# Kernel tuning notes

Measured on AMD Instinct MI355X. Metric: run time of the kernel, lower is better.

The kernel has to match this reference:

```python
import jax, jax.numpy as jnp
import numpy as np

# model constants (from source: PRE/COMM/OUT sizes; chosen: G, D, E, T, NF)
G, D, E, T = 128, 64, 8, 4096          # group feats, per-elevator feats, n elevators, timesteps
PRE, CI, CH, OUT, NF = 256, 128, 128, 128, 64
ROUNDS, DROPOFF = 3, 0.333
IN = G + D                              # elevator_input_size = 192
OIN = 2 * CH + IN                       # out-LSTM input = 448


def _cell(x, h, c, Wih, Whh, b):
    # torch nn.LSTM cell, gate order i,f,g,o; b = b_ih + b_hh
    g = x @ Wih.T + h @ Whh.T + b
    i, f, gg, o = jnp.split(g, 4, axis=-1)
    c2 = jax.nn.sigmoid(f) * c + jax.nn.sigmoid(i) * jnp.tanh(gg)
    h2 = jax.nn.sigmoid(o) * jnp.tanh(c2)
    return h2, c2


def _forward(features, pre_h0, pre_c0, out_h0, out_c0,
             Wih_p0, Whh_p0, b_p0, Wih_p1, Whh_p1, b_p1, Wfc, bfc,
             Wih_c0, Whh_c0, b_c0, Wih_c1, Whh_c1, b_c1,
             Wih_o, Whh_o, b_o, Wtar, btar, Wdir, bdir):
    def step(carry, feat):
        pre_h, pre_c, out_h, out_c = carry
        group = feat[:G]
        ele = feat[G:].reshape(E, D)
        x = jnp.concatenate([jnp.broadcast_to(group, (E, G)), ele], axis=-1)  # [E, IN]
        # preprocess: 2-layer LSTM single step, batched over elevators
        h0, c0 = _cell(x, pre_h[:, 0], pre_c[:, 0], Wih_p0, Whh_p0, b_p0)
        h1, c1 = _cell(h0, pre_h[:, 1], pre_c[:, 1], Wih_p1, Whh_p1, b_p1)
        pre_out = jax.nn.leaky_relu(h1 @ Wfc.T + bfc, 0.05)                   # [E, CI]
        new_pre_h = jnp.stack([h0, h1], axis=1)
        new_pre_c = jnp.stack([c0, c1], axis=1)
        # alpha-decayed communication rounds: sequential scan over elevators
        ch = jnp.zeros((2, CH), jnp.float32)
        cc = jnp.zeros((2, CH), jnp.float32)
        alpha = 1.0
        for _ in range(ROUNDS):
            def comm_step(cs, xin, alpha=alpha):
                ch_, cc_ = cs
                h0n, c0n = _cell(xin, ch_[0], cc_[0], Wih_c0, Whh_c0, b_c0)
                h0b = (1.0 - alpha) * ch_[0] + alpha * h0n
                c0b = (1.0 - alpha) * cc_[0] + alpha * c0n
                h1n, c1n = _cell(h0b, ch_[1], cc_[1], Wih_c1, Whh_c1, b_c1)
                h1b = (1.0 - alpha) * ch_[1] + alpha * h1n
                c1b = (1.0 - alpha) * cc_[1] + alpha * c1n
                return (jnp.stack([h0b, h1b]), jnp.stack([c0b, c1b])), None
            (ch, cc), _ = jax.lax.scan(comm_step, (ch, cc), pre_out)
            alpha *= DROPOFF
        group_dec = cc.reshape(-1)                                            # [2*CH] = comm_c.flatten()
        out_in = jnp.concatenate([jnp.broadcast_to(group_dec, (E, 2 * CH)), x], axis=-1)  # [E, OIN]
        oh, oc = _cell(out_in, out_h, out_c, Wih_o, Whh_o, b_o)
        tar = jax.nn.softmax(oh @ Wtar.T + btar, axis=-1)                     # [E, NF]
        dr = jax.nn.softmax(oh @ Wdir.T + bdir, axis=-1)                      # [E, 3]
        return (new_pre_h, new_pre_c, oh, oc), (tar, dr)

    _, (tar_seq, dir_seq) = jax.lax.scan(step, (pre_h0, pre_c0, out_h0, out_c0), features)
    return tar_seq, dir_seq


def setup_inputs() -> dict:
    key = jax.random.key(0)
    ks = iter(jax.random.split(key, 32))
    p = lambda *s: jax.random.normal(next(ks), s, jnp.float32) * 0.05
    return {
        "features": jax.random.normal(next(ks), (T, G + E * D), jnp.float32),
        "pre_h0": jnp.zeros((E, 2, PRE), jnp.float32),
        "pre_c0": jnp.zeros((E, 2, PRE), jnp.float32),
        "out_h0": jnp.zeros((E, OUT), jnp.float32),
        "out_c0": jnp.zeros((E, OUT), jnp.float32),
        "Wih_p0": p(4 * PRE, IN), "Whh_p0": p(4 * PRE, PRE), "b_p0": p(4 * PRE),
        "Wih_p1": p(4 * PRE, PRE), "Whh_p1": p(4 * PRE, PRE), "b_p1": p(4 * PRE),
        "Wfc": p(CI, PRE), "bfc": p(CI),
        "Wih_c0": p(4 * CH, CI), "Whh_c0": p(4 * CH, CH), "b_c0": p(4 * CH),
        "Wih_c1": p(4 * CH, CH), "Whh_c1": p(4 * CH, CH), "b_c1": p(4 * CH),
        "Wih_o": p(4 * OUT, OIN), "Whh_o": p(4 * OUT, OUT), "b_o": p(4 * OUT),
        "Wtar": p(NF, OUT), "btar": p(NF),
        "Wdir": p(3, OUT), "bdir": p(3),
    }


def reference(features, pre_h0, pre_c0, out_h0, out_c0,
              Wih_p0, Whh_p0, b_p0, Wih_p1, Whh_p1, b_p1, Wfc, bfc,
              Wih_c0, Whh_c0, b_c0, Wih_c1, Whh_c1, b_c1,
              Wih_o, Whh_o, b_o, Wtar, btar, Wdir, bdir):
    return _forward(features, pre_h0, pre_c0, out_h0, out_c0,
                    Wih_p0, Whh_p0, b_p0, Wih_p1, Whh_p1, b_p1, Wfc, bfc,
                    Wih_c0, Whh_c0, b_c0, Wih_c1, Whh_c1, b_c1,
                    Wih_o, Whh_o, b_o, Wtar, btar, Wdir, bdir)
```

## Files before the change

### kernel.cpp

```cpp
#include <hip/hip_runtime.h>
#include <hip/hip_bf16.h>

#define T_   4096
#define E_   8
#define NCON 176

typedef unsigned long long ull;

__device__ __forceinline__ float sigm(float x)  { return 1.0f / (1.0f + __expf(-x)); }
__device__ __forceinline__ float tanh_(float x) { return 1.0f - 2.0f / (__expf(2.0f * x) + 1.0f); }

__device__ __forceinline__ ull aload64(const ull* p) {
  return __hip_atomic_load(p, __ATOMIC_RELAXED, __HIP_MEMORY_SCOPE_AGENT);
}
__device__ __forceinline__ int aload32(const int* p) {
  return __hip_atomic_load(p, __ATOMIC_RELAXED, __HIP_MEMORY_SCOPE_AGENT);
}
__device__ __forceinline__ float aloadf(const float* p) {
  return __hip_atomic_load(p, __ATOMIC_RELAXED, __HIP_MEMORY_SCOPE_AGENT);
}
__device__ __forceinline__ void lbar() {
  asm volatile("s_waitcnt lgkmcnt(0)\n\ts_barrier" ::: "memory");
}

#define FMA_8(ACC, W, VA, VB)                                   \
  ACC[0] = fmaf((W), (VA).x, ACC[0]); ACC[1] = fmaf((W), (VA).y, ACC[1]); \
  ACC[2] = fmaf((W), (VA).z, ACC[2]); ACC[3] = fmaf((W), (VA).w, ACC[3]); \
  ACC[4] = fmaf((W), (VB).x, ACC[4]); ACC[5] = fmaf((W), (VB).y, ACC[5]); \
  ACC[6] = fmaf((W), (VB).z, ACC[6]); ACC[7] = fmaf((W), (VB).w, ACC[7]);

__global__ void initK(const float* __restrict__ Wih_p0, const float* __restrict__ Whh_p0,
                      const float* __restrict__ Wih_p1, const float* __restrict__ Whh_p1,
                      const float* __restrict__ Wih_c0, const float* __restrict__ Whh_c0,
                      const float* __restrict__ Wih_c1, const float* __restrict__ Whh_c1,
                      const float* __restrict__ Wih_o,
                      float* wt_p0, float* wt_p1, float* wt_c0, float* wt_c1,
                      float* wt_o1, float* wt_o2, int* flags) {
  const int NW = 458752 + 524288 + 131072 + 131072 + 131072 + 98304;
  const int NF = 2 * 64 * 32 * 32 + 512 * 32;
  const int NTOT = NW + NF;
  const int gsz = gridDim.x * blockDim.x;
  for (int i = blockIdx.x * blockDim.x + threadIdx.x; i < NTOT; i += gsz) {
    int idx = i;
    if (idx < 458752) { int k = idx >> 10, c = idx & 1023;
      int wg = c >> 5, r5 = c & 31, gate = r5 >> 3, jl = r5 & 7;
      int col = gate * 256 + wg * 8 + jl;
      wt_p0[idx] = (k < 192) ? Wih_p0[col * 192 + k] : Whh_p0[col * 256 + (k - 192)]; continue; }
    idx -= 458752;
    if (idx < 524288) { int k = idx >> 10, c = idx & 1023;
      int wg = c >> 5, r5 = c & 31, gate = r5 >> 3, jl = r5 & 7;
      int col = gate * 256 + wg * 8 + jl;
      wt_p1[idx] = (k < 256) ? Wih_p1[col * 256 + k] : Whh_p1[col * 256 + (k - 256)]; continue; }
    idx -= 524288;
    if (idx < 131072) { int k = idx >> 9, r = idx & 511;
      wt_c0[idx] = (k < 128) ? Wih_c0[r * 128 + k] : Whh_c0[r * 128 + (k - 128)]; continue; }
    idx -= 131072;
    if (idx < 131072) { int k = idx >> 9, r = idx & 511;
      wt_c1[idx] = (k < 128) ? Wih_c1[r * 128 + k] : Whh_c1[r * 128 + (k - 128)]; continue; }
    idx -= 131072;
    if (idx < 131072) { int k = idx >> 9, r = idx & 511;
      wt_o1[idx] = Wih_o[r * 448 + k]; continue; }
    idx -= 131072;
    if (idx < 98304) { int k = idx >> 9, r = idx & 511;
      wt_o2[idx] = Wih_o[r * 448 + 256 + k]; continue; }
    idx -= 98304;
    flags[idx] = 0;
  }
}

__global__ void opre2K(const float* __restrict__ feat, const float* __restrict__ wt_o2,
                       __hip_bfloat16* __restrict__ opre2) {
  __shared__ float xb[192 * 8];
  const int t = blockIdx.x, tid = threadIdx.x;
  const float* ft = feat + (size_t)t * 640;
  for (int idx = tid; idx < 192 * 8; idx += 256) {
    int k = idx >> 3, e = idx & 7;
    xb[idx] = (k < 128) ? ft[k] : ft[128 + e * 64 + (k - 128)];
  }
  __syncthreads();
  const int r = tid;
  float A0[8] = {0,0,0,0,0,0,0,0};
  float A1[8] = {0,0,0,0,0,0,0,0};
  const float4* x4 = (const float4*)xb;
  #pragma unroll 2
  for (int k = 0; k < 192; ++k) {
    float w0 = wt_o2[k * 512 + r];
    float w1 = wt_o2[k * 512 + 256 + r];
    float4 a = x4[k * 2], b = x4[k * 2 + 1];
    FMA_8(A0, w0, a, b);
    FMA_8(A1, w1, a, b);
  }
  #pragma unroll
  for (int e = 0; e < 8; ++e) {
    opre2[((size_t)t * 8 + e) * 512 + r]       = __float2bfloat16(A0[e]);
    opre2[((size_t)t * 8 + e) * 512 + 256 + r] = __float2bfloat16(A1[e]);
  }
}

__device__ __forceinline__ void comm_cell(
    const float* __restrict__ wt, const float* __restrict__ bias,
    const float* xin, float* hL, float* cL, float* glb, float* hout,
    float alpha, int tid) {
  const int r = tid;
  float A0[8] = {0,0,0,0,0,0,0,0};
  float A1[8] = {0,0,0,0,0,0,0,0};
  const float4* x4 = (const float4*)xin;
  #pragma unroll 2
  for (int k = 0; k < 128; ++k) {
    float w0 = wt[k * 512 + r];
    float w1 = wt[k * 512 + 256 + r];
    float4 a = x4[k * 2], b = x4[k * 2 + 1];
    FMA_8(A0, w0, a, b);
    FMA_8(A1, w1, a, b);
  }
  const float4* h4 = (const float4*)hL;
  #pragma unroll 2
  for (int k = 0; k < 128; ++k) {
    float w0 = wt[(128 + k) * 512 + r];
    float w1 = wt[(128 + k) * 512 + 256 + r];
    float4 a = h4[k * 2], b = h4[k * 2 + 1];
    FMA_8(A0, w0, a, b);
    FMA_8(A1, w1, a, b);
  }
  {
    float4* g4 = (float4*)glb;
    g4[r * 2]             = make_float4(A0[0], A0[1], A0[2], A0[3]);
    g4[r * 2 + 1]         = make_float4(A0[4], A0[5], A0[6], A0[7]);
    g4[(256 + r) * 2]     = make_float4(A1[0], A1[1], A1[2], A1[3]);
    g4[(256 + r) * 2 + 1] = make_float4(A1[4], A1[5], A1[6], A1[7]);
  }
  __syncthreads();
  for (int idx = tid; idx < 1024; idx += 256) {
    int jj = idx >> 3, tt = idx & 7;
    float gi = glb[jj * 8 + tt]         + bias[jj];
    float gf = glb[(128 + jj) * 8 + tt] + bias[128 + jj];
    float gg = glb[(256 + jj) * 8 + tt] + bias[256 + jj];
    float go = glb[(384 + jj) * 8 + tt] + bias[384 + jj];
    float cold = cL[idx], hold = hL[idx];
    float c2 = sigm(gf) * cold + sigm(gi) * tanh_(gg);
    float h2 = sigm(go) * tanh_(c2);
    float hb = fmaf(alpha, h2 - hold, hold);
    float cb = fmaf(alpha, c2 - cold, cold);
    hL[idx] = hb; cL[idx] = cb;
    if (hout) hout[idx] = hb;
  }
  __syncthreads();
}

__launch_bounds__(256, 1)
__global__ void megaK(const float* __restrict__ feat,
                      const float* __restrict__ pre_h0, const float* __restrict__ pre_c0,
                      const float* __restrict__ wt_p0, const float* __restrict__ wt_p1,
                      const float* __restrict__ b_p0, const float* __restrict__ b_p1,
                      float* __restrict__ h0ring, float* __restrict__ h1ring,
                      float* __restrict__ h1all,
                      int* __restrict__ flagsA, int* __restrict__ flagsB,
                      const float* __restrict__ Wfc, const float* __restrict__ bfc,
                      const float* __restrict__ wt_c0, const float* __restrict__ wt_c1,
                      const float* __restrict__ b_c0, const float* __restrict__ b_c1,
                      const float* __restrict__ wt_o1, const float* __restrict__ b_o,
                      float* __restrict__ opre1, int* __restrict__ flagC,
                      const __hip_bfloat16* __restrict__ opre2,
                      const float* __restrict__ Whh_o, const float* __restrict__ out_h0,
                      const float* __restrict__ out_c0, float* __restrict__ oh_g) {
  __shared__ float lds[38912];
  const int wg = blockIdx.x, tid = threadIdx.x;

  if (wg < 32) {
    float* wl   = lds;
    float* xbuf = lds + 14336;
    float* hsf  = lds + 15872;
    float* gl   = lds + 17920;
    const int r5 = tid & 31, kq = tid >> 5;
    for (int idx = tid; idx < 14336; idx += 256)
      wl[idx] = wt_p0[(size_t)(idx >> 5) * 1024 + wg * 32 + (idx & 31)];
    float creg = 0.f, bi = 0.f, bff = 0.f, bg = 0.f, bo = 0.f;
    if (tid < 64) {
      const int jl = tid >> 3, e = tid & 7, j = wg * 8 + jl;
      creg = pre_c0[(e * 2 + 0) * 256 + j];
      bi = b_p0[j]; bff = b_p0[256 + j]; bg = b_p0[512 + j]; bo = b_p0[768 + j];
    }
    for (int idx = tid; idx < 2048; idx += 256) {
      int k = idx >> 3, e = idx & 7;
      hsf[idx] = pre_h0[(e * 2 + 0) * 256 + k];
    }
    for (int idx = tid; idx < 1536; idx += 256) {
      int k = idx >> 3, e = idx & 7;
      xbuf[idx] = (k < 128) ? feat[k] : feat[128 + e * 64 + (k - 128)];
    }
    __syncthreads();
    float Ax[8] = {0,0,0,0,0,0,0,0};
    {
      const float4* x4 = (const float4*)xbuf;
      #pragma unroll
      for (int k = kq * 24; k < kq * 24 + 24; ++k) {
        float w = wl[k * 32 + r5];
        float4 a = x4[k * 2], b = x4[k * 2 + 1];
        FMA_8(Ax, w, a, b);
      }
    }
    for (int t = 0; t < T_; ++t) {
      float px[6];
      if (t + 1 < T_) {
        const float* ft1 = feat + (size_t)(t + 1) * 640;
        #pragma unroll
        for (int i = 0; i < 6; ++i) {
          int idx = tid + i * 256; int k = idx >> 3, e = idx & 7;
          px[i] = (k < 128) ? ft1[k] : ft1[128 + e * 64 + (k - 128)];
        }
      }
      float A[8];
      #pragma unroll
      for (int i = 0; i < 8; ++i) A[i] = Ax[i];
      {
        const float4* h4 = (const float4*)hsf;
        #pragma unroll
        for (int k2 = 0; k2 < 32; ++k2) {
          const int k = kq * 32 + k2;
          float w = wl[(192 + k) * 32 + r5];
          float4 a = h4[k * 2], b = h4[k * 2 + 1];
          FMA_8(A, w, a, b);
        }
      }
      {
        float4* g4 = (float4*)gl;
        g4[(kq * 32 + r5) * 2]     = make_float4(A[0], A[1], A[2], A[3]);
        g4[(kq * 32 + r5) * 2 + 1] = make_float4(A[4], A[5], A[6], A[7]);
      }
      if (tid >= 224 && t >= 8) {
        const int* fp = flagsB + ((size_t)((t - 8) & 63) * 32 + (tid - 224)) * 32;
        while (aload32(fp) < t - 7) __builtin_amdgcn_s_sleep(1);
      }
      lbar();
      if (tid < 64) {
        float s0 = 0.f, s1 = 0.f, s2 = 0.f, s3 = 0.f;
        #pragma unroll
        for (int q = 0; q < 8; ++q) {
          s0 += gl[q * 256 + tid];       s1 += gl[q * 256 + 64 + tid];
          s2 += gl[q * 256 + 128 + tid]; s3 += gl[q * 256 + 192 + tid];
        }
        float c2 = sigm(s1 + bff) * creg + sigm(s0 + bi) * tanh_(s2 + bg);
        float h2 = sigm(s3 + bo) * tanh_(c2);
        creg = c2;
        __hip_atomic_store(&h0ring[(size_t)(t & 7) * 2048 + wg * 64 + tid], h2,
                           __ATOMIC_RELAXED, __HIP_MEMORY_SCOPE_AGENT);
        asm volatile("s_waitcnt vmcnt(0)" ::: "memory");
        if (tid == 0)
          __hip_atomic_store(&flagsA[((size_t)(t & 63) * 32 + wg) * 32], t + 1,
                             __ATOMIC_RELAXED, __HIP_MEMORY_SCOPE_AGENT);
      }
      if (t + 1 >= T_) break;
      #pragma unroll
      for (int i = 0; i < 6; ++i) xbuf[tid + i * 256] = px[i];
      if (tid >= 64 && tid < 96) {
        const int* fp = flagsA + ((size_t)(t & 63) * 32 + (tid - 64)) * 32;
        while (aload32(fp) < t + 1) __builtin_amdgcn_s_sleep(1);
      }
      lbar();
      ull v[4];
      {
        const ull* s8 = (const ull*)(h0ring + (size_t)(t & 7) * 2048);
        #pragma unroll
        for (int i = 0; i < 4; ++i) v[i] = aload64(s8 + tid * 4 + i);
      }
      #pragma unroll
      for (int i = 0; i < 8; ++i) Ax[i] = 0.f;
      {
        const float4* x4 = (const float4*)xbuf;
        #pragma unroll
        for (int k = kq * 24; k < kq * 24 + 24; ++k) {
          float w = wl[k * 32 + r5];
          float4 a = x4[k * 2], b = x4[k * 2 + 1];
          FMA_8(Ax, w, a, b);
        }
      }
      {
        ull* d8 = (ull*)hsf;
        #pragma unroll
        for (int i = 0; i < 4; ++i) d8[tid * 4 + i] = v[i];
      }
      lbar();
    }
  } else if (wg < 64) {
    const int wgl = wg - 32;
    float* wl  = lds;
    float* xh0 = lds + 16384;
    float* hsf = lds + 18432;
    float* gl  = lds + 20480;
    const int r5 = tid & 31, kq = tid >> 5;
    for (int idx = tid; idx < 16384; idx += 256)
      wl[idx] = wt_p1[(size_t)(idx >> 5) * 1024 + wgl * 32 + (idx & 31)];
    float creg = 0.f, bi = 0.f, bff = 0.f, bg = 0.f, bo = 0.f;
    if (tid < 64) {
      const int jl = tid >> 3, e = tid & 7, j = wgl * 8 + jl;
      creg = pre_c0[(e * 2 + 1) * 256 + j];
      bi = b_p1[j]; bff = b_p1[256 + j]; bg = b_p1[512 + j]; bo = b_p1[768 + j];
    }
    for (int idx = tid; idx < 2048; idx += 256) {
      int k = idx >> 3, e = idx & 7;
      hsf[idx] = pre_h0[(e * 2 + 1) * 256 + k];
    }
    __syncthreads();
    if (tid >= 64 && tid < 128) {
      const int lane = tid - 64;
      const int slot = lane >> 5, b = lane & 31;
      const int* fp = flagsA + ((size_t)slot * 32 + b) * 32;
      while (aload32(fp) < slot + 1) __builtin_amdgcn_s_sleep(1);
    }
    __syncthreads();
    ull v0[4];
    {
      const ull* s8 = (const ull*)h0ring;
      #pragma unroll
      for (int i = 0; i < 4; ++i) v0[i] = aload64(s8 + tid * 4 + i);
    }
    {
      ull* d8 = (ull*)xh0;
      #pragma unroll
      for (int i = 0; i < 4; ++i) d8[tid * 4 + i] = v0[i];
    }
    lbar();
    float Ax[8] = {0,0,0,0,0,0,0,0};
    {
      const float4* x4 = (const float4*)xh0;
      #pragma unroll
      for (int k = kq * 32; k < kq * 32 + 32; ++k) {
        float w = wl[k * 32 + r5];
        float4 a = x4[k * 2], b = x4[k * 2 + 1];
        FMA_8(Ax, w, a, b);
      }
    }
    {
      const ull* s8 = (const ull*)(h0ring + 2048);
      #pragma unroll
      for (int i = 0; i < 4; ++i) v0[i] = aload64(s8 + tid * 4 + i);
    }
    for (int t = 0; t < T_; ++t) {
      float A[8];
      #pragma unroll
      for (int i = 0; i < 8; ++i) A[i] = Ax[i];
      {
        const float4* h4 = (const float4*)hsf;
        #pragma unroll
        for (int k2 = 0; k2 < 32; ++k2) {
          const int k = kq * 32 + k2;
          float w = wl[(256 + k) * 32 + r5];
          float4 a = h4[k * 2], b = h4[k * 2 + 1];
          FMA_8(A, w, a, b);
        }
      }
      {
        float4* g4 = (float4*)gl;
        g4[(kq * 32 + r5) * 2]     = make_float4(A[0], A[1], A[2], A[3]);
        g4[(kq * 32 + r5) * 2 + 1] = make_float4(A[4], A[5], A[6], A[7]);
      }
      lbar();
      if (tid < 64) {
        float s0 = 0.f, s1 = 0.f, s2 = 0.f, s3 = 0.f;
        #pragma unroll
        for (int q = 0; q < 8; ++q) {
          s0 += gl[q * 256 + tid];       s1 += gl[q * 256 + 64 + tid];
          s2 += gl[q * 256 + 128 + tid]; s3 += gl[q * 256 + 192 + tid];
        }
        float c2 = sigm(s1 + bff) * creg + sigm(s0 + bi) * tanh_(s2 + bg);
        float h2 = sigm(s3 + bo) * tanh_(c2);
        creg = c2;
        __hip_atomic_store(&h1ring[(size_t)(t & 7) * 2048 + wgl * 64 + tid], h2,
                           __ATOMIC_RELAXED, __HIP_MEMORY_SCOPE_AGENT);
        __hip_atomic_store(&h1all[(size_t)t * 2048 + wgl * 64 + tid], h2,
                           __ATOMIC_RELAXED, __HIP_MEMORY_SCOPE_AGENT);
        asm volatile("s_waitcnt vmcnt(0)" ::: "memory");
        if (tid == 0)
          __hip_atomic_store(&flagsB[((size_t)(t & 63) * 32 + wgl) * 32], t + 1,
                             __ATOMIC_RELAXED, __HIP_MEMORY_SCOPE_AGENT);
      }
      if (t + 1 >= T_) break;
      if (tid >= 64 && tid < 128) {
        const int lane = tid - 64;
        if (lane < 32) {
          const int* fp = flagsB + ((size_t)(t & 63) * 32 + lane) * 32;
          while (aload32(fp) < t + 1) __builtin_amdgcn_s_sleep(1);
        } else if (t + 2 < T_) {
          const int* fp = flagsA + ((size_t)((t + 2) & 63) * 32 + (lane - 32)) * 32;
          while (aload32(fp) < t + 3) __builtin_amdgcn_s_sleep(1);
        }
      }
      lbar();
      ull v1[4];
      {
        const ull* s8 = (const ull*)(h1ring + (size_t)(t & 7) * 2048);
        #pragma unroll
        for (int i = 0; i < 4; ++i) v1[i] = aload64(s8 + tid * 4 + i);
      }
      {
        ull* d8 = (ull*)xh0;
        #pragma unroll
        for (int i = 0; i < 4; ++i) d8[tid * 4 + i] = v0[i];
      }
      lbar();
      if (t + 2 < T_) {
        const ull* s8 = (const ull*)(h0ring + (size_t)((t + 2) & 7) * 2048);
        #pragma unroll
        for (int i = 0; i < 4; ++i) v0[i] = aload64(s8 + tid * 4 + i);
      }
      #pragma unroll
      for (int i = 0; i < 8; ++i) Ax[i] = 0.f;
      {
        const float4* x4 = (const float4*)xh0;
        #pragma unroll
        for (int k = kq * 32; k < kq * 32 + 32; ++k) {
          float w = wl[k * 32 + r5];
          float4 a = x4[k * 2], b = x4[k * 2 + 1];
          FMA_8(Ax, w, a, b);
        }
      }
      {
        ull* d8 = (ull*)hsf;
        #pragma unroll
        for (int i = 0; i < 4; ++i) d8[tid * 4 + i] = v1[i];
      }
      lbar();
    }
  } else if (wg < 72) {
    const int e = wg - 64;
    float* wlds = lds;
    float* ohl  = lds + 32768;
    float* gl   = lds + 32896;
    for (int idx = tid; idx < 32768; idx += 256) {
      int k = idx >> 8, rr = idx & 255;
      wlds[idx] = Whh_o[(256 + rr) * 128 + k];
    }
    float w[128];
    #pragma unroll
    for (int k = 0; k < 128; ++k) w[k] = Whh_o[tid * 128 + k];
    if (tid < 128) ohl[tid] = out_h0[e * 128 + tid];
    float creg = (tid < 128) ? out_c0[e * 128 + tid] : 0.f;
    __syncthreads();
    if (tid == 0) { while (aload32(&flagC[0]) == 0) __builtin_amdgcn_s_sleep(4); }
    __syncthreads();
    const int r0 = tid, r1 = tid + 256;
    float pa = aloadf(&opre1[r0]), pb = aloadf(&opre1[r1]);
    float qa = __bfloat162float(opre2[(size_t)e * 512 + r0]);
    float qb = __bfloat162float(opre2[(size_t)e * 512 + r1]);
    float na = aloadf(&opre1[512 + r0]), nb = aloadf(&opre1[512 + r1]);
    float ma = __bfloat162float(opre2[(size_t)(8 + e) * 512 + r0]);
    float mb = __bfloat162float(opre2[(size_t)(8 + e) * 512 + r1]);
    for (int t = 0; t < T_; ++t) {
      float a0 = pa + qa, a1 = pb + qb;
      pa = na; pb = nb; qa = ma; qb = mb;
      if ((t & 7) == 6 && t + 2 < T_) {
        if (tid == 0) { while (aload32(&flagC[((t + 2) >> 3) * 32]) == 0) __builtin_amdgcn_s_sleep(4); }
        __syncthreads();
      }
      if (t + 2 < T_) {
        na = aloadf(&opre1[(size_t)(t + 2) * 512 + r0]);
        nb = aloadf(&opre1[(size_t)(t + 2) * 512 + r1]);
        ma = __bfloat162float(opre2[((size_t)(t + 2) * 8 + e) * 512 + r0]);
        mb = __bfloat162float(opre2[((size_t)(t + 2) * 8 + e) * 512 + r1]);
      }
      const float4* o4 = (const float4*)ohl;
      #pragma unroll
      for (int kk = 0; kk < 32; ++kk) {
        float4 x = o4[kk];
        a0 = fmaf(w[kk * 4 + 0], x.x, a0); a0 = fmaf(w[kk * 4 + 1], x.y, a0);
        a0 = fmaf(w[kk * 4 + 2], x.z, a0); a0 = fmaf(w[kk * 4 + 3], x.w, a0);
        a1 = fmaf(wlds[(kk * 4 + 0) * 256 + tid], x.x, a1);
        a1 = fmaf(wlds[(kk * 4 + 1) * 256 + tid], x.y, a1);
        a1 = fmaf(wlds[(kk * 4 + 2) * 256 + tid], x.z, a1);
        a1 = fmaf(wlds[(kk * 4 + 3) * 256 + tid], x.w, a1);
      }
      gl[r0] = a0; gl[r1] = a1;
      __syncthreads();
      if (tid < 128) {
        float gi = gl[tid], gf = gl[128 + tid], gg = gl[256 + tid], go = gl[384 + tid];
        float c2 = sigm(gf) * creg + sigm(gi) * tanh_(gg);
        float h2 = sigm(go) * tanh_(c2);
        creg = c2;
        ohl[tid] = h2;
        oh_g[(size_t)t * 1024 + e * 128 + tid] = h2;
      }
      __syncthreads();
    }
  } else {
    const int cb = wg - 72;
    float* h1c    = lds;
    float* polAll = lds + 16384;
    float* ch0 = lds + 24576; float* cc0 = lds + 25600;
    float* ch1 = lds + 26624; float* cc1 = lds + 27648;
    float* h0b = lds + 28672;
    float* glb = lds + 29696;
    for (int chunk = cb; chunk < 512; chunk += NCON) {
      const int t0 = chunk * 8;
      if (tid < 32) {
        const int* fp = flagsB + ((size_t)((t0 + 7) & 63) * 32 + tid) * 32;
        while (aload32(fp) < t0 + 8) __builtin_amdgcn_s_sleep(4);
      }
      __syncthreads();
      {
        const ull* src = (const ull*)(h1all + (size_t)t0 * 2048);
        ull* dst = (ull*)h1c;
        for (int i = tid; i < 8192; i += 256) dst[i] = aload64(src + i);
      }
      __syncthreads();
      {
        const int c = tid >> 1, half = tid & 1;
        const float bv = bfc[c];
        const float* wrow = Wfc + c * 256;
        for (int tt = 0; tt < 8; ++tt) {
          float a0 = bv, a1 = bv, a2 = bv, a3 = bv;
          const float4* h4 = (const float4*)(h1c + tt * 2048);
          #pragma unroll 4
          for (int k = 0; k < 256; ++k) {
            float wv = wrow[k];
            float4 x = h4[k * 2 + half];
            a0 = fmaf(wv, x.x, a0); a1 = fmaf(wv, x.y, a1);
            a2 = fmaf(wv, x.z, a2); a3 = fmaf(wv, x.w, a3);
          }
          float vv[4] = {a0, a1, a2, a3};
          #pragma unroll
          for (int i = 0; i < 4; ++i) {
            float v = vv[i];
            v = (v > 0.f) ? v : 0.05f * v;
            polAll[(half * 4 + i) * 1024 + c * 8 + tt] = v;
          }
        }
      }
      for (int idx = tid; idx < 1024; idx += 256) { ch0[idx]=0.f; cc0[idx]=0.f; ch1[idx]=0.f; cc1[idx]=0.f; }
      __syncthreads();
      float alpha = 1.0f;
      for (int rd = 0; rd < 3; ++rd) {
        for (int e = 0; e < E_; ++e) {
          comm_cell(wt_c0, b_c0, polAll + e * 1024, ch0, cc0, glb, h0b, alpha, tid);
          comm_cell(wt_c1, b_c1, h0b, ch1, cc1, glb, nullptr, alpha, tid);
        }
        alpha *= 0.333f;
      }
      {
        const int r = tid;
        float A0[8], A1[8];
        #pragma unroll
        for (int tt = 0; tt < 8; ++tt) { A0[tt] = b_o[r]; A1[tt] = b_o[256 + r]; }
        const float4* c04 = (const float4*)cc0;
        const float4* c14 = (const float4*)cc1;
        #pragma unroll 2
        for (int k = 0; k < 128; ++k) {
          float w0 = wt_o1[k * 512 + r], w1 = wt_o1[k * 512 + 256 + r];
          float4 a = c04[k * 2], b = c04[k * 2 + 1];
          FMA_8(A0, w0, a, b);
          FMA_8(A1, w1, a, b);
        }
        #pragma unroll 2
        for (int k = 0; k < 128; ++k) {
          float w0 = wt_o1[(128 + k) * 512 + r], w1 = wt_o1[(128 + k) * 512 + 256 + r];
          float4 a = c14[k * 2], b = c14[k * 2 + 1];
          FMA_8(A0, w0, a, b);
          FMA_8(A1, w1, a, b);
        }
        #pragma unroll
        for (int tt = 0; tt < 8; ++tt) {
          __hip_atomic_store(&opre1[((size_t)(t0 + tt)) * 512 + r], A0[tt],
                             __ATOMIC_RELAXED, __HIP_MEMORY_SCOPE_AGENT);
          __hip_atomic_store(&opre1[((size_t)(t0 + tt)) * 512 + 256 + r], A1[tt],
                             __ATOMIC_RELAXED, __HIP_MEMORY_SCOPE_AGENT);
        }
      }
      __syncthreads();
      if (tid == 0)
        __hip_atomic_store(&flagC[chunk * 32], 1, __ATOMIC_RELAXED, __HIP_MEMORY_SCOPE_AGENT);
      __syncthreads();
    }
  }
}

__global__ void phaseD(const float* __restrict__ oh_g,
                       const float* __restrict__ Wtar, const float* __restrict__ btar,
                       const float* __restrict__ Wdir, const float* __restrict__ bdir,
                       float* __restrict__ outp) {
  __shared__ float ohl[1024];
  const int t = blockIdx.x, tid = threadIdx.x;
  for (int idx = tid; idx < 1024; idx += 64) ohl[idx] = oh_g[(size_t)t * 1024 + idx];
  __syncthreads();
  const int f = tid;
  for (int e = 0; e < E_; ++e) {
    float acc = btar[f];
    const float* wr = Wtar + f * 128;
    #pragma unroll 4
    for (int k = 0; k < 128; ++k) acc = fmaf(wr[k], ohl[e * 128 + k], acc);
    float m = acc;
    #pragma unroll
    for (int off = 32; off; off >>= 1) m = fmaxf(m, __shfl_xor(m, off, 64));
    float ex = __expf(acc - m);
    float s = ex;
    #pragma unroll
    for (int off = 32; off; off >>= 1) s += __shfl_xor(s, off, 64);
    outp[((size_t)t * 8 + e) * 64 + f] = ex / s;
  }
  if (tid < 8) {
    int e = tid;
    float d0 = bdir[0], d1 = bdir[1], d2 = bdir[2];
    #pragma unroll 4
    for (int k = 0; k < 128; ++k) {
      float x = ohl[e * 128 + k];
      d0 = fmaf(Wdir[k], x, d0);
      d1 = fmaf(Wdir[128 + k], x, d1);
      d2 = fmaf(Wdir[256 + k], x, d2);
    }
    float m = fmaxf(d0, fmaxf(d1, d2));
    float x0 = __expf(d0 - m), x1 = __expf(d1 - m), x2 = __expf(d2 - m);
    float s = x0 + x1 + x2;
    float* dp = outp + (size_t)T_ * 8 * 64 + ((size_t)t * 8 + e) * 3;
    dp[0] = x0 / s; dp[1] = x1 / s; dp[2] = x2 / s;
  }
}

extern "C" void kernel_launch(void* const* d_in, const int* in_sizes, int n_in,
                              void* d_out, int out_size, void* d_ws, size_t ws_size,
                              hipStream_t stream) {
  (void)in_sizes; (void)n_in; (void)out_size; (void)ws_size;
  const float* feat   = (const float*)d_in[0];
  const float* pre_h0 = (const float*)d_in[1];
  const float* pre_c0 = (const float*)d_in[2];
  const float* out_h0 = (const float*)d_in[3];
  const float* out_c0 = (const float*)d_in[4];
  const float* Wih_p0 = (const float*)d_in[5];
  const float* Whh_p0 = (const float*)d_in[6];
  const float* b_p0   = (const float*)d_in[7];
  const float* Wih_p1 = (const float*)d_in[8];
  const float* Whh_p1 = (const float*)d_in[9];
  const float* b_p1   = (const float*)d_in[10];
  const float* Wfc    = (const float*)d_in[11];
  const float* bfc    = (const float*)d_in[12];
  const float* Wih_c0 = (const float*)d_in[13];
  const float* Whh_c0 = (const float*)d_in[14];
  const float* b_c0   = (const float*)d_in[15];
  const float* Wih_c1 = (const float*)d_in[16];
  const float* Whh_c1 = (const float*)d_in[17];
  const float* b_c1   = (const float*)d_in[18];
  const float* Wih_o  = (const float*)d_in[19];
  const float* Whh_o  = (const float*)d_in[20];
  const float* b_o    = (const float*)d_in[21];
  const float* Wtar   = (const float*)d_in[22];
  const float* btar   = (const float*)d_in[23];
  const float* Wdir   = (const float*)d_in[24];
  const float* bdir   = (const float*)d_in[25];
  float* outp = (float*)d_out;

  float* ws = (float*)d_ws;
  size_t off = 0;
  float* opre1    = ws + off; off += (size_t)T_ * 512;
  float* oh_g     = ws + off; off += (size_t)T_ * E_ * 128;
  float* wt_p0    = ws + off; off += (size_t)448 * 1024;
  float* wt_p1    = ws + off; off += (size_t)512 * 1024;
  float* wt_c0    = ws + off; off += (size_t)256 * 512;
  float* wt_c1    = ws + off; off += (size_t)256 * 512;
  float* wt_o1    = ws + off; off += (size_t)256 * 512;
  float* wt_o2    = ws + off; off += (size_t)192 * 512;
  __hip_bfloat16* opre2 = (__hip_bfloat16*)(ws + off);
  off += (size_t)T_ * E_ * 512 / 2;
  float* h1all  = ws + off; off += (size_t)T_ * 2048;
  float* h0ring = ws + off; off += (size_t)8 * 2048;
  float* h1ring = ws + off; off += (size_t)8 * 2048;
  int* flags    = (int*)(ws + off);
  int* flagsA   = flags;
  int* flagsB   = flags + (size_t)64 * 32 * 32;
  int* flagC    = flags + (size_t)2 * 64 * 32 * 32;

  initK<<<dim3(1024), dim3(256), 0, stream>>>(
      Wih_p0, Whh_p0, Wih_p1, Whh_p1, Wih_c0, Whh_c0, Wih_c1, Whh_c1, Wih_o,
      wt_p0, wt_p1, wt_c0, wt_c1, wt_o1, wt_o2, flags);
  opre2K<<<dim3(T_), dim3(256), 0, stream>>>(feat, wt_o2, opre2);
  megaK<<<dim3(32 + 32 + 8 + NCON), dim3(256), 0, stream>>>(
      feat, pre_h0, pre_c0, wt_p0, wt_p1, b_p0, b_p1,
      h0ring, h1ring, h1all, flagsA, flagsB,
      Wfc, bfc, wt_c0, wt_c1, b_c0, b_c1, wt_o1, b_o, opre1, flagC,
      opre2, Whh_o, out_h0, out_c0, oh_g);
  phaseD<<<dim3(T_), dim3(64), 0, stream>>>(oh_g, Wtar, btar, Wdir, bdir, outp);
}
```

Before: 16.66 ms.

## Replace per-step flag handshakes with sequence-tagged ring entries between LSTM layers

Each h value written to the inter-workgroup rings is packed with its timestep tag in a 64-bit word, so consumers poll the data itself instead of waiting on separate flagsA counters. The vmcnt drain and flag store after every step disappear, and each block skips reloading its own slice by writing it straight to LDS. The h0 ring grows to 32 slots and the layer-1 backpressure flag is published only every 8 steps, loosening the coupling between producers and consumers. This doubles ring traffic and relies on 64-bit atomic loads being untorn and on the wider ring staying ahead of readers.

```diff
diff --git a/kernel.cpp b/kernel.cpp
--- a/kernel.cpp
+++ b/kernel.cpp
@@ -35,10 +35,10 @@
                       const float* __restrict__ Wih_c1, const float* __restrict__ Whh_c1,
                       const float* __restrict__ Wih_o,
                       float* wt_p0, float* wt_p1, float* wt_c0, float* wt_c1,
-                      float* wt_o1, float* wt_o2, int* flags) {
+                      float* wt_o1, float* wt_o2, int* zbase) {
   const int NW = 458752 + 524288 + 131072 + 131072 + 131072 + 98304;
-  const int NF = 2 * 64 * 32 * 32 + 512 * 32;
-  const int NTOT = NW + NF;
+  const int NZ = 131072 + 32768 + 65536 + 16384;
+  const int NTOT = NW + NZ;
   const int gsz = gridDim.x * blockDim.x;
   for (int i = blockIdx.x * blockDim.x + threadIdx.x; i < NTOT; i += gsz) {
     int idx = i;
@@ -64,7 +64,7 @@
     if (idx < 98304) { int k = idx >> 9, r = idx & 511;
       wt_o2[idx] = Wih_o[r * 448 + 256 + k]; continue; }
     idx -= 98304;
-    flags[idx] = 0;
+    zbase[idx] = 0;
   }
 }
 
@@ -152,9 +152,9 @@
                       const float* __restrict__ pre_h0, const float* __restrict__ pre_c0,
                       const float* __restrict__ wt_p0, const float* __restrict__ wt_p1,
                       const float* __restrict__ b_p0, const float* __restrict__ b_p1,
-                      float* __restrict__ h0ring, float* __restrict__ h1ring,
+                      ull* __restrict__ h0ring, ull* __restrict__ h1ring,
                       float* __restrict__ h1all,
-                      int* __restrict__ flagsA, int* __restrict__ flagsB,
+                      int* __restrict__ flagsB,
                       const float* __restrict__ Wfc, const float* __restrict__ bfc,
                       const float* __restrict__ wt_c0, const float* __restrict__ wt_c1,
                       const float* __restrict__ b_c0, const float* __restrict__ b_c1,
@@ -189,6 +189,7 @@
       xbuf[idx] = (k < 128) ? feat[k] : feat[128 + e * 64 + (k - 128)];
     }
     __syncthreads();
+    const bool own = ((tid >> 3) == wg);
     float Ax[8] = {0,0,0,0,0,0,0,0};
     {
       const float4* x4 = (const float4*)xbuf;
@@ -227,9 +228,10 @@
         g4[(kq * 32 + r5) * 2]     = make_float4(A[0], A[1], A[2], A[3]);
         g4[(kq * 32 + r5) * 2 + 1] = make_float4(A[4], A[5], A[6], A[7]);
       }
-      if (tid >= 224 && t >= 8) {
-        const int* fp = flagsB + ((size_t)((t - 8) & 63) * 32 + (tid - 224)) * 32;
-        while (aload32(fp) < t - 7) __builtin_amdgcn_s_sleep(1);
+      if (t >= 24 && tid >= 224) {
+        const int t2 = (t - 24) | 7;
+        const int* fp = flagsB + ((size_t)(t2 & 63) * 32 + (tid - 224)) * 32;
+        while (aload32(fp) < t2 + 1) __builtin_amdgcn_s_sleep(1);
       }
       lbar();
       if (tid < 64) {
@@ -242,26 +244,20 @@
         float c2 = sigm(s1 + bff) * creg + sigm(s0 + bi) * tanh_(s2 + bg);
         float h2 = sigm(s3 + bo) * tanh_(c2);
         creg = c2;
-        __hip_atomic_store(&h0ring[(size_t)(t & 7) * 2048 + wg * 64 + tid], h2,
+        ull pk = ((ull)(unsigned)(t + 1) << 32) | (ull)__float_as_uint(h2);
+        __hip_atomic_store(&h0ring[(size_t)(t & 31) * 2048 + wg * 64 + tid], pk,
                            __ATOMIC_RELAXED, __HIP_MEMORY_SCOPE_AGENT);
-        asm volatile("s_waitcnt vmcnt(0)" ::: "memory");
-        if (tid == 0)
-          __hip_atomic_store(&flagsA[((size_t)(t & 63) * 32 + wg) * 32], t + 1,
-                             __ATOMIC_RELAXED, __HIP_MEMORY_SCOPE_AGENT);
+        hsf[wg * 64 + tid] = h2;
       }
       if (t + 1 >= T_) break;
       #pragma unroll
       for (int i = 0; i < 6; ++i) xbuf[tid + i * 256] = px[i];
-      if (tid >= 64 && tid < 96) {
-        const int* fp = flagsA + ((size_t)(t & 63) * 32 + (tid - 64)) * 32;
-        while (aload32(fp) < t + 1) __builtin_amdgcn_s_sleep(1);
-      }
       lbar();
-      ull v[4];
-      {
-        const ull* s8 = (const ull*)(h0ring + (size_t)(t & 7) * 2048);
-        #pragma unroll
-        for (int i = 0; i < 4; ++i) v[i] = aload64(s8 + tid * 4 + i);
+      ull v[8];
+      const ull* rp = h0ring + (size_t)(t & 31) * 2048 + tid * 8;
+      if (!own) {
+        #pragma unroll
+        for (int i = 0; i < 8; ++i) v[i] = aload64(rp + i);
       }
       #pragma unroll
       for (int i = 0; i < 8; ++i) Ax[i] = 0.f;
@@ -274,10 +270,24 @@
           FMA_8(Ax, w, a, b);
         }
       }
-      {
-        ull* d8 = (ull*)hsf;
-        #pragma unroll
-        for (int i = 0; i < 4; ++i) d8[tid * 4 + i] = v[i];
+      if (!own) {
+        const unsigned want = (unsigned)(t + 1);
+        while (true) {
+          bool ok = true;
+          #pragma unroll
+          for (int i = 0; i < 8; ++i) ok &= ((unsigned)(v[i] >> 32) == want);
+          if (ok) break;
+          __builtin_amdgcn_s_sleep(1);
+          #pragma unroll
+          for (int i = 0; i < 8; ++i) v[i] = aload64(rp + i);
+        }
+        float4* h4w = (float4*)hsf;
+        h4w[tid * 2] = make_float4(
+            __uint_as_float((unsigned)v[0]), __uint_as_float((unsigned)v[1]),
+            __uint_as_float((unsigned)v[2]), __uint_as_float((unsigned)v[3]));
+        h4w[tid * 2 + 1] = make_float4(
+            __uint_as_float((unsigned)v[4]), __uint_as_float((unsigned)v[5]),
+            __uint_as_float((unsigned)v[6]), __uint_as_float((unsigned)v[7]));
       }
       lbar();
     }
@@ -301,23 +311,28 @@
       hsf[idx] = pre_h0[(e * 2 + 1) * 256 + k];
     }
     __syncthreads();
-    if (tid >= 64 && tid < 128) {
-      const int lane = tid - 64;
-      const int slot = lane >> 5, b = lane & 31;
-      const int* fp = flagsA + ((size_t)slot * 32 + b) * 32;
-      while (aload32(fp) < slot + 1) __builtin_amdgcn_s_sleep(1);
-    }
-    __syncthreads();
-    ull v0[4];
+    const bool own = ((tid >> 3) == wgl);
+    float pv[8];
     {
-      const ull* s8 = (const ull*)h0ring;
-      #pragma unroll
-      for (int i = 0; i < 4; ++i) v0[i] = aload64(s8 + tid * 4 + i);
-    }
-    {
-      ull* d8 = (ull*)xh0;
-      #pragma unroll
-      for (int i = 0; i < 4; ++i) d8[tid * 4 + i] = v0[i];
+      ull v[8];
+      const ull* rp = h0ring + tid * 8;
+      #pragma unroll
+      for (int i = 0; i < 8; ++i) v[i] = aload64(rp + i);
+      while (true) {
+        bool ok = true;
+        #pragma unroll
+        for (int i = 0; i < 8; ++i) ok &= ((unsigned)(v[i] >> 32) == 1u);
+        if (ok) break;
+        __builtin_amdgcn_s_sleep(1);
+        #pragma unroll
+        for (int i = 0; i < 8; ++i) v[i] = aload64(rp + i);
+      }
+      ((float4*)xh0)[tid * 2] = make_float4(
+          __uint_as_float((unsigned)v[0]), __uint_as_float((unsigned)v[1]),
+          __uint_as_float((unsigned)v[2]), __uint_as_float((unsigned)v[3]));
+      ((float4*)xh0)[tid * 2 + 1] = make_float4(
+          __uint_as_float((unsigned)v[4]), __uint_as_float((unsigned)v[5]),
+          __uint_as_float((unsigned)v[6]), __uint_as_float((unsigned)v[7]));
     }
     lbar();
     float Ax[8] = {0,0,0,0,0,0,0,0};
@@ -331,9 +346,21 @@
       }
     }
     {
-      const ull* s8 = (const ull*)(h0ring + 2048);
-      #pragma unroll
-      for (int i = 0; i < 4; ++i) v0[i] = aload64(s8 + tid * 4 + i);
+      ull v[8];
+      const ull* rp = h0ring + 2048 + tid * 8;
+      #pragma unroll
+      for (int i = 0; i < 8; ++i) v[i] = aload64(rp + i);
+      while (true) {
+        bool ok = true;
+        #pragma unroll
+        for (int i = 0; i < 8; ++i) ok &= ((unsigned)(v[i] >> 32) == 2u);
+        if (ok) break;
+        __builtin_amdgcn_s_sleep(1);
+        #pragma unroll
+        for (int i = 0; i < 8; ++i) v[i] = aload64(rp + i);
+      }
+      #pragma unroll
+      for (int i = 0; i < 8; ++i) pv[i] = __uint_as_float((unsigned)v[i]);
     }
     for (int t = 0; t < T_; ++t) {
       float A[8];
@@ -365,43 +392,34 @@
         float c2 = sigm(s1 + bff) * creg + sigm(s0 + bi) * tanh_(s2 + bg);
         float h2 = sigm(s3 + bo) * tanh_(c2);
         creg = c2;
-        __hip_atomic_store(&h1ring[(size_t)(t & 7) * 2048 + wgl * 64 + tid], h2,
+        ull pk = ((ull)(unsigned)(t + 1) << 32) | (ull)__float_as_uint(h2);
+        __hip_atomic_store(&h1ring[(size_t)(t & 7) * 2048 + wgl * 64 + tid], pk,
                            __ATOMIC_RELAXED, __HIP_MEMORY_SCOPE_AGENT);
         __hip_atomic_store(&h1all[(size_t)t * 2048 + wgl * 64 + tid], h2,
                            __ATOMIC_RELAXED, __HIP_MEMORY_SCOPE_AGENT);
-        asm volatile("s_waitcnt vmcnt(0)" ::: "memory");
-        if (tid == 0)
-          __hip_atomic_store(&flagsB[((size_t)(t & 63) * 32 + wgl) * 32], t + 1,
-                             __ATOMIC_RELAXED, __HIP_MEMORY_SCOPE_AGENT);
+        hsf[wgl * 64 + tid] = h2;
+        if ((t & 7) == 7) {
+          asm volatile("s_waitcnt vmcnt(0)" ::: "memory");
+          if (tid == 0)
+            __hip_atomic_store(&flagsB[((size_t)(t & 63) * 32 + wgl) * 32], t + 1,
+                               __ATOMIC_RELAXED, __HIP_MEMORY_SCOPE_AGENT);
+        }
       }
       if (t + 1 >= T_) break;
-      if (tid >= 64 && tid < 128) {
-        const int lane = tid - 64;
-        if (lane < 32) {
-          const int* fp = flagsB + ((size_t)(t & 63) * 32 + lane) * 32;
-          while (aload32(fp) < t + 1) __builtin_amdgcn_s_sleep(1);
-        } else if (t + 2 < T_) {
-          const int* fp = flagsA + ((size_t)((t + 2) & 63) * 32 + (lane - 32)) * 32;
-          while (aload32(fp) < t + 3) __builtin_amdgcn_s_sleep(1);
-        }
-      }
+      ((float4*)xh0)[tid * 2]     = make_float4(pv[0], pv[1], pv[2], pv[3]);
+      ((float4*)xh0)[tid * 2 + 1] = make_float4(pv[4], pv[5], pv[6], pv[7]);
       lbar();
-      ull v1[4];
-      {
-        const ull* s8 = (const ull*)(h1ring + (size_t)(t & 7) * 2048);
-        #pragma unroll
-        for (int i = 0; i < 4; ++i) v1[i] = aload64(s8 + tid * 4 + i);
-      }
-      {
-        ull* d8 = (ull*)xh0;
-        #pragma unroll
-        for (int i = 0; i < 4; ++i) d8[tid * 4 + i] = v0[i];
-      }
-      lbar();
-      if (t + 2 < T_) {
-        const ull* s8 = (const ull*)(h0ring + (size_t)((t + 2) & 7) * 2048);
-        #pragma unroll
-        for (int i = 0; i < 4; ++i) v0[i] = aload64(s8 + tid * 4 + i);
+      ull w1[8], w0[8];
+      const ull* rph1 = h1ring + (size_t)(t & 7) * 2048 + tid * 8;
+      if (!own) {
+        #pragma unroll
+        for (int i = 0; i < 8; ++i) w1[i] = aload64(rph1 + i);
+      }
+      const bool have0 = (t + 2 < T_);
+      const ull* rph0 = h0ring + (size_t)((t + 2) & 31) * 2048 + tid * 8;
+      if (have0) {
+        #pragma unroll
+        for (int i = 0; i < 8; ++i) w0[i] = aload64(rph0 + i);
       }
       #pragma unroll
       for (int i = 0; i < 8; ++i) Ax[i] = 0.f;
@@ -414,10 +432,38 @@
           FMA_8(Ax, w, a, b);
         }
       }
-      {
-        ull* d8 = (ull*)hsf;
-        #pragma unroll
-        for (int i = 0; i < 4; ++i) d8[tid * 4 + i] = v1[i];
+      if (!own) {
+        const unsigned want = (unsigned)(t + 1);
+        while (true) {
+          bool ok = true;
+          #pragma unroll
+          for (int i = 0; i < 8; ++i) ok &= ((unsigned)(w1[i] >> 32) == want);
+          if (ok) break;
+          __builtin_amdgcn_s_sleep(1);
+          #pragma unroll
+          for (int i = 0; i < 8; ++i) w1[i] = aload64(rph1 + i);
+        }
+        float4* h4w = (float4*)hsf;
+        h4w[tid * 2] = make_float4(
+            __uint_as_float((unsigned)w1[0]), __uint_as_float((unsigned)w1[1]),
+            __uint_as_float((unsigned)w1[2]), __uint_as_float((unsigned)w1[3]));
+        h4w[tid * 2 + 1] = make_float4(
+            __uint_as_float((unsigned)w1[4]), __uint_as_float((unsigned)w1[5]),
+            __uint_as_float((unsigned)w1[6]), __uint_as_float((unsigned)w1[7]));
+      }
+      if (have0) {
+        const unsigned want = (unsigned)(t + 3);
+        while (true) {
+          bool ok = true;
+          #pragma unroll
+          for (int i = 0; i < 8; ++i) ok &= ((unsigned)(w0[i] >> 32) == want);
+          if (ok) break;
+          __builtin_amdgcn_s_sleep(1);
+          #pragma unroll
+          for (int i = 0; i < 8; ++i) w0[i] = aload64(rph0 + i);
+        }
+        #pragma unroll
+        for (int i = 0; i < 8; ++i) pv[i] = __uint_as_float((unsigned)w0[i]);
       }
       lbar();
     }
@@ -658,20 +704,20 @@
   __hip_bfloat16* opre2 = (__hip_bfloat16*)(ws + off);
   off += (size_t)T_ * E_ * 512 / 2;
   float* h1all  = ws + off; off += (size_t)T_ * 2048;
-  float* h0ring = ws + off; off += (size_t)8 * 2048;
-  float* h1ring = ws + off; off += (size_t)8 * 2048;
+  ull* h0ring   = (ull*)(ws + off); off += (size_t)32 * 2048 * 2;
+  ull* h1ring   = (ull*)(ws + off); off += (size_t)8 * 2048 * 2;
   int* flags    = (int*)(ws + off);
-  int* flagsA   = flags;
-  int* flagsB   = flags + (size_t)64 * 32 * 32;
-  int* flagC    = flags + (size_t)2 * 64 * 32 * 32;
+  int* flagsB   = flags;
+  int* flagC    = flags + (size_t)64 * 32 * 32;
+  int* zbase    = (int*)h0ring;
 
   initK<<<dim3(1024), dim3(256), 0, stream>>>(
       Wih_p0, Whh_p0, Wih_p1, Whh_p1, Wih_c0, Whh_c0, Wih_c1, Whh_c1, Wih_o,
-      wt_p0, wt_p1, wt_c0, wt_c1, wt_o1, wt_o2, flags);
+      wt_p0, wt_p1, wt_c0, wt_c1, wt_o1, wt_o2, zbase);
   opre2K<<<dim3(T_), dim3(256), 0, stream>>>(feat, wt_o2, opre2);
   megaK<<<dim3(32 + 32 + 8 + NCON), dim3(256), 0, stream>>>(
       feat, pre_h0, pre_c0, wt_p0, wt_p1, b_p0, b_p1,
-      h0ring, h1ring, h1all, flagsA, flagsB,
+      h0ring, h1ring, h1all, flagsB,
       Wfc, bfc, wt_c0, wt_c1, b_c0, b_c1, wt_o1, b_o, opre1, flagC,
       opre2, Whh_o, out_h0, out_c0, oh_g);
   phaseD<<<dim3(T_), dim3(64), 0, stream>>>(oh_g, Wtar, btar, Wdir, bdir, outp);
```

New measurement: 19.59 ms. 1.18x slower.
